# Kernel optimization log

Measured on AMD Instinct MI355X. Metric: run time of the kernel, lower is better.

Reference implementation:

```python
import jax, jax.numpy as jnp
import numpy as np

N_HEADS = 16
EPS = 1e-5

def _ln(h, g, b):
    mu = jnp.mean(h, axis=-1, keepdims=True)
    var = jnp.var(h, axis=-1, keepdims=True)
    return (h - mu) * jax.lax.rsqrt(var + EPS) * g + b

def setup_inputs() -> dict:
    key = jax.random.key(0)
    ks = jax.random.split(key, 8)
    B, S, D, M = 2, 2048, 2048, 8192
    x = jax.random.normal(ks[0], (B, S, D), dtype=jnp.float32)
    # causal mask: True where attention is disallowed (j > i)
    mask = jnp.triu(jnp.ones((S, S), dtype=bool), k=1)[None, None]
    s = 1.0 / np.sqrt(D)
    Wq = jax.random.normal(ks[1], (D, D), dtype=jnp.float32) * s
    Wk = jax.random.normal(ks[2], (D, D), dtype=jnp.float32) * s
    Wv = jax.random.normal(ks[3], (D, D), dtype=jnp.float32) * s
    Wo = jax.random.normal(ks[4], (D, D), dtype=jnp.float32) * s
    W1 = jax.random.normal(ks[5], (D, M), dtype=jnp.float32) * s
    b1 = jnp.zeros((M,), dtype=jnp.float32)
    W2 = jax.random.normal(ks[6], (M, D), dtype=jnp.float32) * (1.0 / np.sqrt(M))
    b2 = jnp.zeros((D,), dtype=jnp.float32)
    ln1_g = jnp.ones((D,), jnp.float32); ln1_b = jnp.zeros((D,), jnp.float32)
    ln2_g = jnp.ones((D,), jnp.float32); ln2_b = jnp.zeros((D,), jnp.float32)
    return dict(x=x, self_attn_mask=mask, Wq=Wq, Wk=Wk, Wv=Wv, Wo=Wo,
                ln1_g=ln1_g, ln1_b=ln1_b, W1=W1, b1=b1, W2=W2, b2=b2,
                ln2_g=ln2_g, ln2_b=ln2_b)

def reference(x, self_attn_mask, Wq, Wk, Wv, Wo, ln1_g, ln1_b, W1, b1, W2, b2, ln2_g, ln2_b):
    B, S, D = x.shape
    n = N_HEADS
    d = D // n
    # --- self-attention with pre-norm residual ---
    h = _ln(x, ln1_g, ln1_b)
    # NOTE: source uses .view(b, n_heads, i, head_dim) with NO transpose -> plain reshape
    q = (h @ Wq).reshape(B, n, S, d)
    k = (h @ Wk).reshape(B, n, S, d)
    v = (h @ Wv).reshape(B, n, S, d)
    score = jnp.einsum('bnid,bnjd->bnij', q, k)
    # NOTE: source masks BEFORE scaling, so -1e9 is also divided by sqrt(d)
    score = jnp.where(self_attn_mask, jnp.float32(-1e9), score) / jnp.sqrt(jnp.float32(d))
    w = jax.nn.softmax(score, axis=3)
    o = jnp.einsum('bnij,bnjd->bnid', w, v)
    o = o.transpose(0, 2, 1, 3).reshape(B, S, D)  # b n i d -> b i (n d)
    x = x + o @ Wo
    # --- FFN with pre-norm residual ---
    h2 = _ln(x, ln2_g, ln2_b)
    ff = jnp.maximum(h2 @ W1 + b1, 0.0) @ W2 + b2
    return x + ff
```

## Files before the change

### kernel.cpp

```cpp
#include <hip/hip_runtime.h>
#include <cstdint>

using bf16x8 = __attribute__((ext_vector_type(8))) short;
using f32x4  = __attribute__((ext_vector_type(4))) float;

__device__ __forceinline__ unsigned short f2bf(float f) {
  union { float f; unsigned u; } v; v.f = f;
  unsigned u = v.u;
  u += 0x7fffu + ((u >> 16) & 1u);
  return (unsigned short)(u >> 16);
}

__device__ __forceinline__ void gload_lds16(const unsigned short* g, unsigned short* l) {
  __builtin_amdgcn_global_load_lds(
      (const __attribute__((address_space(1))) unsigned int*)g,
      (__attribute__((address_space(3))) unsigned int*)l, 16, 0, 0);
}

__global__ __launch_bounds__(256) void ln_kernel(
    const float* __restrict__ x, const float* __restrict__ g,
    const float* __restrict__ bb, unsigned short* __restrict__ h)
{
  const int D = 2048;
  const int row = blockIdx.x;
  const float* xr = x + (size_t)row * D;
  const int t = threadIdx.x;
  float4 v0 = ((const float4*)xr)[t];
  float4 v1 = ((const float4*)xr)[t + 256];
  float s  = v0.x+v0.y+v0.z+v0.w + v1.x+v1.y+v1.z+v1.w;
  float ss = v0.x*v0.x+v0.y*v0.y+v0.z*v0.z+v0.w*v0.w
           + v1.x*v1.x+v1.y*v1.y+v1.z*v1.z+v1.w*v1.w;
  #pragma unroll
  for (int off = 1; off < 64; off <<= 1) {
    s  += __shfl_xor(s, off);
    ss += __shfl_xor(ss, off);
  }
  __shared__ float red[8];
  const int wave = t >> 6, lane = t & 63;
  if (lane == 0) { red[wave] = s; red[4+wave] = ss; }
  __syncthreads();
  s  = red[0]+red[1]+red[2]+red[3];
  ss = red[4]+red[5]+red[6]+red[7];
  const float mu   = s * (1.f/2048.f);
  const float var  = ss * (1.f/2048.f) - mu*mu;
  const float rstd = rsqrtf(var + 1e-5f);
  unsigned short* hr = h + (size_t)row * D;
  #pragma unroll
  for (int q = 0; q < 2; ++q) {
    float4 v = q ? v1 : v0;
    int vecidx = t + q*256;
    float4 gg  = ((const float4*)g)[vecidx];
    float4 bv  = ((const float4*)bb)[vecidx];
    ushort4 o;
    o.x = f2bf((v.x-mu)*rstd*gg.x + bv.x);
    o.y = f2bf((v.y-mu)*rstd*gg.y + bv.y);
    o.z = f2bf((v.z-mu)*rstd*gg.z + bv.z);
    o.w = f2bf((v.w-mu)*rstd*gg.w + bv.w);
    *(ushort4*)(hr + vecidx*4) = o;
  }
}

__global__ __launch_bounds__(256) void transpose_cast(
    const float* __restrict__ W, unsigned short* __restrict__ WT,
    int K, int N)
{
  __shared__ float tile[32][33];
  const int tx = threadIdx.x, ty = threadIdx.y;
  const int n0 = blockIdx.x * 32, k0 = blockIdx.y * 32;
  #pragma unroll
  for (int r = 0; r < 4; ++r)
    tile[ty + r*8][tx] = W[(size_t)(k0 + ty + r*8) * N + n0 + tx];
  __syncthreads();
  #pragma unroll
  for (int r = 0; r < 4; ++r)
    WT[(size_t)(n0 + ty + r*8) * K + k0 + tx] = f2bf(tile[tx][ty + r*8]);
}

template<int BM, bool BIAS, bool RELU, bool RESID, bool OUTBF16>
__global__ __launch_bounds__(512, 2) void gemm8(
    const unsigned short* __restrict__ A, const unsigned short* __restrict__ BT,
    const float* __restrict__ bias, const float* __restrict__ resid,
    void* __restrict__ Cp, int M, int N, int K, int nbx)
{
  constexpr int BN = 256, BK = 64;
  constexpr int MPH = BM / 64;
  constexpr int AQ  = BM / 64;
  constexpr int LPK = AQ + 4;
  __shared__ __align__(16) unsigned short lds[2][(BM + BN) * BK];

  const int tid  = threadIdx.x;
  const int lane = tid & 63, wave = tid >> 6;
  const int l15 = lane & 15, lh = lane >> 4;
  const int wr = wave >> 2, wc = wave & 3;

  const int nwg = gridDim.x;
  const int q8  = nwg >> 3;
  const int wg  = blockIdx.x;
  const int swz = (wg & 7) * q8 + (wg >> 3);
  const size_t bm = (size_t)(swz / nbx) * BM;
  const size_t bn = (size_t)(swz % nbx) * BN;
  const int nk = K >> 6;

  auto stageA = [&](int buf, int kt, int qq) {
    int idx = qq * 512 + tid;
    int row = idx >> 3, c = idx & 7, gc = c ^ (row & 7);
    gload_lds16(A + (bm + row) * (size_t)K + (size_t)kt * BK + gc * 8,
                &lds[buf][0] + idx * 8);
  };
  auto stageB = [&](int buf, int kt, int qq) {
    int idx = qq * 512 + tid;
    int row = idx >> 3, c = idx & 7, gc = c ^ (row & 7);
    gload_lds16(BT + (bn + row) * (size_t)K + (size_t)kt * BK + gc * 8,
                &lds[buf][BM * BK] + idx * 8);
  };

  f32x4 acc[MPH * 2][4] = {};

  #pragma unroll
  for (int qq = 0; qq < AQ; ++qq) stageA(0, 0, qq);
  #pragma unroll
  for (int qq = 0; qq < 4; ++qq)  stageB(0, 0, qq);
  #pragma unroll
  for (int qq = 0; qq < AQ; ++qq) stageA(1, 1, qq);
  #pragma unroll
  for (int qq = 0; qq < 4; ++qq)  stageB(1, 1, qq);

  for (int kt = 0; kt < nk; ++kt) {
    const int buf = kt & 1;
    if (kt < nk - 1) asm volatile("s_waitcnt vmcnt(%0)" :: "i"(LPK) : "memory");
    else             asm volatile("s_waitcnt vmcnt(0)" ::: "memory");
    __builtin_amdgcn_s_barrier();
    asm volatile("" ::: "memory");

    const unsigned short* La = &lds[buf][0];
    const unsigned short* Lb = &lds[buf][BM * BK];
    bf16x8 bfr[2][4];
    const bool pf = (kt + 2 < nk);

    #pragma unroll
    for (int p = 0; p < MPH; ++p) {
      if (p > 0 && pf) {
        if (MPH == 4) { stageA(buf, kt + 2, p - 1); stageB(buf, kt + 2, p - 1); }
        else          { stageA(buf, kt + 2, 0);
                        stageB(buf, kt + 2, 0); stageB(buf, kt + 2, 1); }
      }
      if (p == 0) {
        #pragma unroll
        for (int kk = 0; kk < 2; ++kk)
          #pragma unroll
          for (int n = 0; n < 4; ++n) {
            int brow = wc * 64 + n * 16 + l15;
            bfr[kk][n] = *(const bf16x8*)(Lb + brow * 64 +
                           ((kk * 32 + lh * 8) ^ ((brow & 7) << 3)));
          }
      }
      bf16x8 af[2][2];
      #pragma unroll
      for (int mi = 0; mi < 2; ++mi) {
        int arow = (p * 4 + wr * 2 + mi) * 16 + l15;
        #pragma unroll
        for (int kk = 0; kk < 2; ++kk)
          af[mi][kk] = *(const bf16x8*)(La + arow * 64 +
                         ((kk * 32 + lh * 8) ^ ((arow & 7) << 3)));
      }
      asm volatile("" ::: "memory");
      __builtin_amdgcn_s_barrier();
      __builtin_amdgcn_s_setprio(1);
      #pragma unroll
      for (int mi = 0; mi < 2; ++mi)
        #pragma unroll
        for (int n = 0; n < 4; ++n)
          #pragma unroll
          for (int kk = 0; kk < 2; ++kk)
            acc[p*2+mi][n] = __builtin_amdgcn_mfma_f32_16x16x32_bf16(
                af[mi][kk], bfr[kk][n], acc[p*2+mi][n], 0, 0, 0);
      __builtin_amdgcn_s_setprio(0);
      asm volatile("" ::: "memory");
      __builtin_amdgcn_s_barrier();
    }
    if (pf) {
      if (MPH == 4) { stageA(buf, kt + 2, 3); stageB(buf, kt + 2, 3); }
      else          { stageA(buf, kt + 2, 1);
                      stageB(buf, kt + 2, 2); stageB(buf, kt + 2, 3); }
    }
  }

  float bv[4];
  if (BIAS) {
    #pragma unroll
    for (int n = 0; n < 4; ++n) bv[n] = bias[bn + wc*64 + n*16 + l15];
  }
  #pragma unroll
  for (int p = 0; p < MPH; ++p) {
    #pragma unroll
    for (int mi = 0; mi < 2; ++mi) {
      #pragma unroll
      for (int r = 0; r < 4; ++r) {
        size_t rrow = bm + (size_t)(p*4 + wr*2 + mi)*16 + lh*4 + r;
        #pragma unroll
        for (int n = 0; n < 4; ++n) {
          size_t ccol = bn + wc*64 + n*16 + l15;
          float v = acc[p*2+mi][n][r];
          if (BIAS)  v += bv[n];
          if (RELU)  v = fmaxf(v, 0.f);
          if (RESID) v += resid[rrow*(size_t)N + ccol];
          if (OUTBF16) ((unsigned short*)Cp)[rrow*(size_t)N + ccol] = f2bf(v);
          else         ((float*)Cp)[rrow*(size_t)N + ccol] = v;
        }
      }
    }
  }
}

__global__ __launch_bounds__(256) void attn_kernel(
    const unsigned short* __restrict__ QKV, unsigned short* __restrict__ O)
{
  constexpr float SCALE = 0.08838834764831845f;
  __shared__ __align__(16) unsigned short Kl[64*128];
  __shared__ __align__(16) unsigned short Vf[64*128];
  __shared__ __align__(16) unsigned short Pl[4*1024];
  const int bid = blockIdx.x;
  const int qt = 31 - (bid >> 5);
  const int nh = bid & 15;
  const int b  = (bid >> 4) & 1;
  const int t = threadIdx.x;
  const int lane = t & 63, wave = t >> 6;
  const int l15 = lane & 15, lh = lane >> 4;
  const int i0 = qt*64 + wave*16;
  const size_t RS = 6144;
  const size_t base = (size_t)b * 2048 * RS;

  const unsigned short* qrow = QKV + base + (size_t)(nh*128 + (i0 >> 4)) * RS;
  bf16x8 qf[4];
  #pragma unroll
  for (int c = 0; c < 4; ++c)
    qf[c] = *(const bf16x8*)(qrow + l15*128 + c*32 + lh*8);

  f32x4 of[8] = {};
  float mrun[4], lrun[4];
  #pragma unroll
  for (int r = 0; r < 4; ++r) { mrun[r] = -INFINITY; lrun[r] = 0.f; }

  const int nkt = qt + 1;
  bf16x8 kr[4], vr[4];
  auto loadKV = [&](int kt) {
    #pragma unroll
    for (int q = 0; q < 4; ++q) {
      int c = t + q*256;
      int j = c >> 4, dd0 = (c & 15) * 8;
      const size_t grow = base + (size_t)(nh*128 + kt*4 + (j >> 4)) * RS + (j & 15)*128 + dd0;
      kr[q] = *(const bf16x8*)(QKV + grow + 2048);
      vr[q] = *(const bf16x8*)(QKV + grow + 4096);
    }
  };
  loadKV(0);

  for (int kt = 0; kt < nkt; ++kt) {
    __syncthreads();
    #pragma unroll
    for (int q = 0; q < 4; ++q) {
      int c = t + q*256;
      int j = c >> 4, dd0 = (c & 15) * 8;
      *(bf16x8*)((char*)Kl + ((j*256 + dd0*2) ^ ((j & 7) << 4))) = kr[q];
      int ks = j >> 5, jq = j & 31;
      int cc = dd0 >> 4;
      int wb = ks*8192 + cc*1024 + (((dd0 & 15) + 16*((jq >> 3) & 3)) & ~7)*16 + (jq & 7)*2;
      #pragma unroll
      for (int e = 0; e < 8; ++e)
        *(unsigned short*)((char*)Vf + wb + ((e ^ cc) * 16)) = (unsigned short)vr[q][e];
    }
    __syncthreads();
    if (kt + 1 < nkt) loadKV(kt + 1);

    f32x4 sc[4] = {};
    #pragma unroll
    for (int jt = 0; jt < 4; ++jt) {
      int row = jt*16 + l15;
      const char* kb = (const char*)Kl + row*256;
      const int sw = (row & 7) << 4;
      #pragma unroll
      for (int c = 0; c < 4; ++c) {
        bf16x8 kf = *(const bf16x8*)(kb + ((c*64 + lh*16) ^ sw));
        sc[jt] = __builtin_amdgcn_mfma_f32_16x16x32_bf16(qf[c], kf, sc[jt], 0, 0, 0);
      }
    }

    float fac[4];
    char* pw = (char*)Pl + wave*2048;
    #pragma unroll
    for (int r = 0; r < 4; ++r) {
      float s0 = sc[0][r]*SCALE, s1 = sc[1][r]*SCALE, s2 = sc[2][r]*SCALE, s3 = sc[3][r]*SCALE;
      if (kt == qt) {
        const int i = i0 + lh*4 + r;
        const int j = kt*64 + l15;
        s0 = (j      > i) ? -INFINITY : s0;
        s1 = (j + 16 > i) ? -INFINITY : s1;
        s2 = (j + 32 > i) ? -INFINITY : s2;
        s3 = (j + 48 > i) ? -INFINITY : s3;
      }
      float mx = fmaxf(fmaxf(s0, s1), fmaxf(s2, s3));
      #pragma unroll
      for (int mk = 1; mk < 16; mk <<= 1) mx = fmaxf(mx, __shfl_xor(mx, mk));
      const float mnew = fmaxf(mrun[r], mx);
      float p0 = __expf(s0 - mnew), p1 = __expf(s1 - mnew);
      float p2 = __expf(s2 - mnew), p3 = __expf(s3 - mnew);
      float psum = (p0 + p1) + (p2 + p3);
      #pragma unroll
      for (int mk = 1; mk < 16; mk <<= 1) psum += __shfl_xor(psum, mk);
      fac[r]  = __expf(mrun[r] - mnew);
      lrun[r] = lrun[r]*fac[r] + psum;
      mrun[r] = mnew;
      const int io = lh*4 + r;
      const int swp = (io & 7) << 4;
      char* pr = pw + io*128;
      *(unsigned short*)(pr + ((     l15*2) ^ swp)) = f2bf(p0);
      *(unsigned short*)(pr + ((32 + l15*2) ^ swp)) = f2bf(p1);
      *(unsigned short*)(pr + ((64 + l15*2) ^ swp)) = f2bf(p2);
      *(unsigned short*)(pr + ((96 + l15*2) ^ swp)) = f2bf(p3);
    }
    #pragma unroll
    for (int c = 0; c < 8; ++c)
      #pragma unroll
      for (int r = 0; r < 4; ++r)
        of[c][r] *= fac[r];

    const char* prd = pw + l15*128;
    const int psw = (l15 & 7) << 4;
    bf16x8 pa0 = *(const bf16x8*)(prd + ((     lh*16) ^ psw));
    bf16x8 pa1 = *(const bf16x8*)(prd + ((64 + lh*16) ^ psw));

    #pragma unroll
    for (int c = 0; c < 8; ++c) {
      const char* vb = (const char*)Vf + c*1024 + ((lane ^ c) * 16);
      bf16x8 v0 = *(const bf16x8*)(vb);
      bf16x8 v1 = *(const bf16x8*)(vb + 8192);
      of[c] = __builtin_amdgcn_mfma_f32_16x16x32_bf16(pa0, v0, of[c], 0, 0, 0);
      of[c] = __builtin_amdgcn_mfma_f32_16x16x32_bf16(pa1, v1, of[c], 0, 0, 0);
    }
  }

  unsigned short* orow = O + ((size_t)(b*2048 + i0))*2048 + nh*128;
  #pragma unroll
  for (int r = 0; r < 4; ++r) {
    const float inv = 1.f / lrun[r];
    #pragma unroll
    for (int c = 0; c < 8; ++c)
      orow[(size_t)(lh*4 + r)*2048 + c*16 + l15] = f2bf(of[c][r]*inv);
  }
}

extern "C" void kernel_launch(void* const* d_in, const int* in_sizes, int n_in,
                              void* d_out, int out_size, void* d_ws, size_t ws_size,
                              hipStream_t stream)
{
  const float* x    = (const float*)d_in[0];
  const float* Wq   = (const float*)d_in[2];
  const float* Wk   = (const float*)d_in[3];
  const float* Wv   = (const float*)d_in[4];
  const float* Wo   = (const float*)d_in[5];
  const float* ln1g = (const float*)d_in[6];
  const float* ln1b = (const float*)d_in[7];
  const float* W1   = (const float*)d_in[8];
  const float* b1   = (const float*)d_in[9];
  const float* W2   = (const float*)d_in[10];
  const float* b2   = (const float*)d_in[11];
  const float* ln2g = (const float*)d_in[12];
  const float* ln2b = (const float*)d_in[13];
  float* out = (float*)d_out;

  char* ws = (char*)d_ws;
  unsigned short* WqkvT  = (unsigned short*)(ws);
  unsigned short* WoT    = (unsigned short*)(ws + 25165824);
  unsigned short* W1T    = (unsigned short*)(ws + 33554432);
  unsigned short* W2T    = (unsigned short*)(ws + 67108864);
  unsigned short* h      = (unsigned short*)(ws + 100663296);
  float*          x2     = (float*)(ws + 117440512);
  unsigned short* QKV    = (unsigned short*)(ws + 150994944);
  unsigned short* attn_o = (unsigned short*)(ws + 201326592);
  unsigned short* ff1    = (unsigned short*)(ws + 150994944);

  dim3 tb(32, 8);
  transpose_cast<<<dim3(64, 64),  tb, 0, stream>>>(Wq, WqkvT,                2048, 2048);
  transpose_cast<<<dim3(64, 64),  tb, 0, stream>>>(Wk, WqkvT + 2048*2048,    2048, 2048);
  transpose_cast<<<dim3(64, 64),  tb, 0, stream>>>(Wv, WqkvT + 2*2048*2048,  2048, 2048);
  transpose_cast<<<dim3(64, 64),  tb, 0, stream>>>(Wo, WoT,                  2048, 2048);
  transpose_cast<<<dim3(256, 64), tb, 0, stream>>>(W1, W1T,                  2048, 8192);
  transpose_cast<<<dim3(64, 256), tb, 0, stream>>>(W2, W2T,                  8192, 2048);

  ln_kernel<<<4096, 256, 0, stream>>>(x, ln1g, ln1b, h);
  gemm8<256,false,false,false,true><<<384, 512, 0, stream>>>(
      h, WqkvT, nullptr, nullptr, QKV, 4096, 6144, 2048, 24);
  attn_kernel<<<1024, 256, 0, stream>>>(QKV, attn_o);
  gemm8<128,false,false,true,false><<<256, 512, 0, stream>>>(
      attn_o, WoT, nullptr, x, x2, 4096, 2048, 2048, 8);
  ln_kernel<<<4096, 256, 0, stream>>>(x2, ln2g, ln2b, h);
  gemm8<256,true,true,false,true><<<512, 512, 0, stream>>>(
      h, W1T, b1, nullptr, ff1, 4096, 8192, 2048, 32);
  gemm8<128,true,false,true,false><<<256, 512, 0, stream>>>(
      ff1, W2T, b2, x2, out, 4096, 2048, 8192, 8);
}
```

Measured before the change: 626.5 us.

## Split-K the FFN down-projection GEMM and move prefetch after LDS reads

The final W2 GEMM (K=8192) now uses BM=256 tiles with a 2-way split-K. Each split writes fp32 partials into workspace, and a new reduce kernel sums the two partials with the bias and residual. The GEMM mainloop also drops one barrier per phase and issues the next-stage global-to-LDS loads after the fragment reads rather than before them. The goal is better wave balance for the 256-tile GEMM through larger tiles, and less sync overhead. The cost is an extra 64 MB of fp32 partial traffic, an extra launch, and a possible LDS race if the barrier removal is unsafe.

```diff
diff --git a/kernel.cpp b/kernel.cpp
--- a/kernel.cpp
+++ b/kernel.cpp
@@ -76,11 +76,32 @@
     WT[(size_t)(n0 + ty + r*8) * K + k0 + tx] = f2bf(tile[tx][ty + r*8]);
 }
 
+__global__ __launch_bounds__(256) void reduce_splitk(
+    const float* __restrict__ P, const float* __restrict__ x2,
+    const float* __restrict__ b2, float* __restrict__ out)
+{
+  const size_t MN4 = (size_t)4096 * 2048 / 4;
+  const float4* P0 = (const float4*)P;
+  const float4* P1 = P0 + MN4;
+  const float4* X  = (const float4*)x2;
+  const float4* B  = (const float4*)b2;
+  for (size_t i = (size_t)blockIdx.x * 256 + threadIdx.x; i < MN4;
+       i += (size_t)gridDim.x * 256) {
+    float4 a = P0[i], b = P1[i], c = X[i], bb = B[i & 511];
+    float4 o;
+    o.x = a.x + b.x + c.x + bb.x;
+    o.y = a.y + b.y + c.y + bb.y;
+    o.z = a.z + b.z + c.z + bb.z;
+    o.w = a.w + b.w + c.w + bb.w;
+    ((float4*)out)[i] = o;
+  }
+}
+
 template<int BM, bool BIAS, bool RELU, bool RESID, bool OUTBF16>
 __global__ __launch_bounds__(512, 2) void gemm8(
     const unsigned short* __restrict__ A, const unsigned short* __restrict__ BT,
     const float* __restrict__ bias, const float* __restrict__ resid,
-    void* __restrict__ Cp, int M, int N, int K, int nbx)
+    void* __restrict__ Cp, int M, int N, int K, int kdepth, int nbx, int ntiles)
 {
   constexpr int BN = 256, BK = 64;
   constexpr int MPH = BM / 64;
@@ -97,9 +118,13 @@
   const int q8  = nwg >> 3;
   const int wg  = blockIdx.x;
   const int swz = (wg & 7) * q8 + (wg >> 3);
-  const size_t bm = (size_t)(swz / nbx) * BM;
-  const size_t bn = (size_t)(swz % nbx) * BN;
-  const int nk = K >> 6;
+  const int split = swz / ntiles;
+  const int tile  = swz % ntiles;
+  const size_t bm = (size_t)(tile / nbx) * BM;
+  const size_t bn = (size_t)(tile % nbx) * BN;
+  A  += (size_t)split * kdepth;
+  BT += (size_t)split * kdepth;
+  const int nk = kdepth >> 6;
 
   auto stageA = [&](int buf, int kt, int qq) {
     int idx = qq * 512 + tid;
@@ -139,11 +164,6 @@
 
     #pragma unroll
     for (int p = 0; p < MPH; ++p) {
-      if (p > 0 && pf) {
-        if (MPH == 4) { stageA(buf, kt + 2, p - 1); stageB(buf, kt + 2, p - 1); }
-        else          { stageA(buf, kt + 2, 0);
-                        stageB(buf, kt + 2, 0); stageB(buf, kt + 2, 1); }
-      }
       if (p == 0) {
         #pragma unroll
         for (int kk = 0; kk < 2; ++kk)
@@ -163,8 +183,11 @@
           af[mi][kk] = *(const bf16x8*)(La + arow * 64 +
                          ((kk * 32 + lh * 8) ^ ((arow & 7) << 3)));
       }
-      asm volatile("" ::: "memory");
-      __builtin_amdgcn_s_barrier();
+      if (p > 0 && pf) {
+        if (MPH == 4) { stageA(buf, kt + 2, p - 1); stageB(buf, kt + 2, p - 1); }
+        else          { stageA(buf, kt + 2, 0);
+                        stageB(buf, kt + 2, 0); stageB(buf, kt + 2, 1); }
+      }
       __builtin_amdgcn_s_setprio(1);
       #pragma unroll
       for (int mi = 0; mi < 2; ++mi)
@@ -190,6 +213,8 @@
     #pragma unroll
     for (int n = 0; n < 4; ++n) bv[n] = bias[bn + wc*64 + n*16 + l15];
   }
+  unsigned short* Cb = (unsigned short*)Cp + (size_t)split * M * N;
+  float*          Cf = (float*)Cp + (size_t)split * M * N;
   #pragma unroll
   for (int p = 0; p < MPH; ++p) {
     #pragma unroll
@@ -204,8 +229,8 @@
           if (BIAS)  v += bv[n];
           if (RELU)  v = fmaxf(v, 0.f);
           if (RESID) v += resid[rrow*(size_t)N + ccol];
-          if (OUTBF16) ((unsigned short*)Cp)[rrow*(size_t)N + ccol] = f2bf(v);
-          else         ((float*)Cp)[rrow*(size_t)N + ccol] = v;
+          if (OUTBF16) Cb[rrow*(size_t)N + ccol] = f2bf(v);
+          else         Cf[rrow*(size_t)N + ccol] = v;
         }
       }
     }
@@ -378,6 +403,7 @@
   unsigned short* QKV    = (unsigned short*)(ws + 150994944);
   unsigned short* attn_o = (unsigned short*)(ws + 201326592);
   unsigned short* ff1    = (unsigned short*)(ws + 150994944);
+  float*          Pws    = (float*)(ws);
 
   dim3 tb(32, 8);
   transpose_cast<<<dim3(64, 64),  tb, 0, stream>>>(Wq, WqkvT,                2048, 2048);
@@ -389,13 +415,14 @@
 
   ln_kernel<<<4096, 256, 0, stream>>>(x, ln1g, ln1b, h);
   gemm8<256,false,false,false,true><<<384, 512, 0, stream>>>(
-      h, WqkvT, nullptr, nullptr, QKV, 4096, 6144, 2048, 24);
+      h, WqkvT, nullptr, nullptr, QKV, 4096, 6144, 2048, 2048, 24, 384);
   attn_kernel<<<1024, 256, 0, stream>>>(QKV, attn_o);
   gemm8<128,false,false,true,false><<<256, 512, 0, stream>>>(
-      attn_o, WoT, nullptr, x, x2, 4096, 2048, 2048, 8);
+      attn_o, WoT, nullptr, x, x2, 4096, 2048, 2048, 2048, 8, 256);
   ln_kernel<<<4096, 256, 0, stream>>>(x2, ln2g, ln2b, h);
   gemm8<256,true,true,false,true><<<512, 512, 0, stream>>>(
-      h, W1T, b1, nullptr, ff1, 4096, 8192, 2048, 32);
-  gemm8<128,true,false,true,false><<<256, 512, 0, stream>>>(
-      ff1, W2T, b2, x2, out, 4096, 2048, 8192, 8);
-}
+      h, W1T, b1, nullptr, ff1, 4096, 8192, 2048, 2048, 32, 512);
+  gemm8<256,false,false,false,false><<<256, 512, 0, stream>>>(
+      ff1, W2T, nullptr, nullptr, Pws, 4096, 2048, 8192, 4096, 8, 128);
+  reduce_splitk<<<2048, 256, 0, stream>>>(Pws, x2, b2, out);
+}
```

Result: no change. 628.7 us (+0.4%).
